# Kernel optimization log

Measured on AMD Instinct MI355X. Metric: run time of the kernel, lower is better.

Reference implementation:

```python
import jax, jax.numpy as jnp
import numpy as np

ALPHA = 1.0
BETA = 0.25
NUM_EMBEDS = 8192
EMBED_DIM = 512
B, T = 32, 256


def setup_inputs() -> dict:
    key = jax.random.key(0)
    k1, k2 = jax.random.split(key)
    z_e = jax.random.normal(k1, (B, EMBED_DIM, T), dtype=jnp.float32)
    codebook = jax.random.normal(k2, (NUM_EMBEDS, EMBED_DIM), dtype=jnp.float32)
    return {"z_e": z_e, "codebook": codebook}


def reference(z_e, codebook):
    # z_e: (b, d, t) -> (b, t, d)
    z = jnp.transpose(z_e, (0, 2, 1))
    b, t, d = z.shape
    flat = z.reshape(-1, d)  # (N, d), N = b*t

    # squared euclidean distances to every codebook vector: (N, K)
    dists = (
        jnp.sum(flat * flat, axis=1, keepdims=True)
        + jnp.sum(codebook * codebook, axis=1)
        - 2.0 * flat @ codebook.T
    )
    idx = jnp.argmin(dists, axis=1)  # (N,)

    # codebook lookup (equivalent to one-hot @ codebook)
    z_q = codebook[idx].reshape(b, t, d)

    # commitment loss (codebook is EMA-updated, so only e_latent term)
    e_latent_loss = jnp.mean((jax.lax.stop_gradient(z_q) - z) ** 2)
    vq_loss = ALPHA * BETA * e_latent_loss

    # straight-through estimator
    z_q_st = z + jax.lax.stop_gradient(z_q - z)
    z_q_out = jnp.transpose(z_q_st, (0, 2, 1))  # back to (b, d, t)

    # perplexity from mean one-hot assignment probabilities
    counts = jnp.zeros((codebook.shape[0],), dtype=jnp.float32).at[idx].add(1.0)
    avg_probs = counts / flat.shape[0]
    perplexity = jnp.exp(-jnp.sum(avg_probs * jnp.log(avg_probs + 1e-10)))

    return z_q_out, vq_loss, perplexity
```

## Files before the change

### kernel.cpp

```cpp
#include <hip/hip_runtime.h>
#include <stdint.h>

typedef _Float16 half8 __attribute__((ext_vector_type(8)));
typedef float floatx16 __attribute__((ext_vector_type(16)));
typedef unsigned long long u64;

#define ALPHA_ 1.0f
#define BETA_ 0.25f
#define NUM_EMBEDS 8192
#define EMBED_DIM 512
#define B_ 32
#define T_ 256
#define N_TOK 8192
#define THR_GAP 0.01f


typedef __attribute__((address_space(1))) const void ga_void;
typedef __attribute__((address_space(3))) void ls_void;
__device__ __forceinline__ void gl_lds16(const void* g, void* l) {
    __builtin_amdgcn_global_load_lds((ga_void*)g, (ls_void*)l, 16, 0, 0);
}

__device__ __forceinline__ uint32_t mono(float s) {
    uint32_t u = __float_as_uint(s);
    return (u & 0x80000000u) ? ~u : (u | 0x80000000u);
}
__device__ __forceinline__ float unmono(uint32_t v) {
    return __uint_as_float((v & 0x80000000u) ? (v ^ 0x80000000u) : ~v);
}

__global__ void pack_kernel(const float* __restrict__ cb, const float* __restrict__ z,
                            _Float16* __restrict__ cb_i, _Float16* __restrict__ zt_i,
                            float* __restrict__ cnorm, u64* __restrict__ wexact,
                            int* __restrict__ counts, float* __restrict__ sse,
                            int* __restrict__ nflag) {
    const int bx = blockIdx.x;
    const int tid = threadIdx.x;
    if (bx < 2048) {
        int row = bx * 4 + (tid >> 6);
        int lane = tid & 63;
        const float* src = cb + (size_t)row * EMBED_DIM + lane * 8;
        float4 v0 = *(const float4*)src;
        float4 v1 = *(const float4*)(src + 4);
        float x[8] = {v0.x, v0.y, v0.z, v0.w, v1.x, v1.y, v1.z, v1.w};
        half8 hh, mm;
        float s = 0.f;
#pragma unroll
        for (int j = 0; j < 8; ++j) {
            s += x[j] * x[j];
            _Float16 hv = (_Float16)x[j];
            hh[j] = hv;
            mm[j] = (_Float16)(x[j] - (float)hv);
        }
        _Float16* dst = cb_i + (size_t)row * 1024 + (lane >> 1) * 32 + (lane & 1) * 8;
        *(half8*)dst = hh;
        *(half8*)(dst + 16) = mm;
#pragma unroll
        for (int d = 32; d; d >>= 1) s += __shfl_xor(s, d, 64);
        if (lane == 0) cnorm[row] = s;
    } else if (bx < 2176) {
        int bz = bx - 2048;
        int lane = tid & 63, ds = tid >> 6;
        int b = bz >> 2;
        int t = ((bz & 3) << 6) + lane;
        size_t n = (size_t)b * T_ + t;
        for (int g = 0; g < 16; ++g) {
            int d0 = g * 32 + ds * 8;
            const float* src = z + ((size_t)b * EMBED_DIM + d0) * T_ + t;
            half8 hh, mm;
#pragma unroll
            for (int j = 0; j < 8; ++j) {
                float x = -2.0f * src[(size_t)j * T_];
                _Float16 hv = (_Float16)x;
                hh[j] = hv;
                mm[j] = (_Float16)(x - (float)hv);
            }
            int gg = g * 4 + ds;
            _Float16* dst = zt_i + n * 1024 + (gg >> 1) * 32 + (gg & 1) * 8;
            *(half8*)dst = hh;
            *(half8*)(dst + 16) = mm;
        }
    } else {
        int i = bx - 2176;
        wexact[i * 256 + tid] = ~0ULL;
        counts[i * 256 + tid] = 0;
        if (i == 0 && tid == 0) { *sse = 0.f; *nflag = 0; }
    }
}

#define MFMA16(a, b, c) __builtin_amdgcn_mfma_f32_32x32x16_f16(a, b, c, 0, 0, 0)

__global__ __launch_bounds__(256, 2) void argmin_kernel(
    const _Float16* __restrict__ cb_i, const _Float16* __restrict__ zt_i,
    const float* __restrict__ cnorm, u64* __restrict__ slot) {
    __shared__ _Float16 smem[24576];
    __shared__ u64 sK[256];
    __shared__ float sV1[256], sV2[256];
    const int tid = threadIdx.x;
    const int l = tid & 63;
    const int wv = tid >> 6;
    const int l31 = l & 31;
    const int hf = l >> 5;
    const int wp = wv >> 1, wq = wv & 1;
    const int n0 = blockIdx.x * 256;
    const int c0 = blockIdx.y * 128;

    const _Float16* gptr[6];
    int lofs[6], bmul[6];
#pragma unroll
    for (int j = 0; j < 6; ++j) {
        int id = wv * 6 + j;
        if (id < 8) {
            int rp = id * 4 + (l >> 4);
            int lid = (l & 15) ^ (rp & 15);
            gptr[j] = cb_i + (size_t)(c0 + (lid >> 2) * 32 + rp) * 1024 + (lid & 3) * 8;
            lofs[j] = id * 512 + l * 8;
            bmul[j] = 4096;
        } else {
            int bid = id - 8;
            int rp = bid * 4 + (l >> 4);
            int lid = (l & 15) ^ (rp & 15);
            gptr[j] = zt_i + (size_t)(n0 + (lid >> 2) * 64 + rp) * 1024 + (lid & 3) * 8;
            lofs[j] = 8192 + bid * 512 + l * 8;
            bmul[j] = 8192;
        }
    }
    auto stagefull = [&](int buf, int ss) {
        const int ga = ss * 32;
#pragma unroll
        for (int j = 0; j < 6; ++j)
            gl_lds16(gptr[j] + ga, smem + lofs[j] + buf * bmul[j]);
    };

    int aoff[2][2], boff[4][2];
#pragma unroll
    for (int pi = 0; pi < 2; ++pi)
#pragma unroll
        for (int p = 0; p < 2; ++p) {
            int lid = (wp * 2 + pi) * 4 + p * 2 + hf;
            aoff[pi][p] = l31 * 128 + (lid ^ (l31 & 15)) * 8;
        }
#pragma unroll
    for (int qi = 0; qi < 4; ++qi)
#pragma unroll
        for (int p = 0; p < 2; ++p) {
            int lid = (wq * 2 + (qi >> 1)) * 4 + p * 2 + hf;
            boff[qi][p] = 8192 + ((qi & 1) * 32 + l31) * 128 + (lid ^ (l31 & 15)) * 8;
        }

    floatx16 acc[2][4];
#pragma unroll
    for (int pi = 0; pi < 2; ++pi)
#pragma unroll
        for (int qi = 0; qi < 4; ++qi)
#pragma unroll
            for (int r = 0; r < 16; ++r) acc[pi][qi][r] = 0.f;

    stagefull(0, 0);
    __syncthreads();
    for (int ss = 0; ss < 32; ++ss) {
        const int buf = ss & 1;
        const int ab = buf * 4096, bb = buf * 8192;
        half8 Ah[2], Am[2], Bh[4], Bm[4];
#pragma unroll
        for (int pi = 0; pi < 2; ++pi) {
            Ah[pi] = *(const half8*)(smem + aoff[pi][0] + ab);
            Am[pi] = *(const half8*)(smem + aoff[pi][1] + ab);
        }
#pragma unroll
        for (int qi = 0; qi < 4; ++qi) {
            Bh[qi] = *(const half8*)(smem + boff[qi][0] + bb);
            Bm[qi] = *(const half8*)(smem + boff[qi][1] + bb);
        }
        if (ss < 31) stagefull(buf ^ 1, ss + 1);
#pragma unroll
        for (int pi = 0; pi < 2; ++pi)
#pragma unroll
            for (int qi = 0; qi < 4; ++qi) {
                acc[pi][qi] = MFMA16(Ah[pi], Bh[qi], acc[pi][qi]);
                acc[pi][qi] = MFMA16(Am[pi], Bh[qi], acc[pi][qi]);
                acc[pi][qi] = MFMA16(Ah[pi], Bm[qi], acc[pi][qi]);
            }
        __syncthreads();
    }

    u64 qk[4];
    float qv1[4], qv2[4];
#pragma unroll
    for (int qi = 0; qi < 4; ++qi) {
        u64 m1k = ~0ULL;
        float m1v = 3.4e38f, m2 = 3.4e38f;
#pragma unroll
        for (int pi = 0; pi < 2; ++pi)
#pragma unroll
            for (int g = 0; g < 4; ++g) {
                const int cb4 = c0 + wp * 64 + pi * 32 + g * 8 + hf * 4;
                float4 cn = *(const float4*)(cnorm + cb4);
                const floatx16& A = acc[pi][qi];
                float sv[4] = {cn.x + A[g * 4 + 0], cn.y + A[g * 4 + 1],
                               cn.z + A[g * 4 + 2], cn.w + A[g * 4 + 3]};
#pragma unroll
                for (int q = 0; q < 4; ++q) {
                    u64 key = ((u64)mono(sv[q]) << 32) | (uint32_t)(cb4 + q);
                    if (key < m1k) { m2 = m1v; m1v = sv[q]; m1k = key; }
                    else m2 = fminf(m2, sv[q]);
                }
            }
        u64 ok = __shfl_xor(m1k, 32, 64);
        float ov = __shfl_xor(m1v, 32, 64);
        float om2 = __shfl_xor(m2, 32, 64);
        if (ok < m1k) { m2 = fminf(fminf(m2, om2), m1v); m1v = ov; m1k = ok; }
        else m2 = fminf(fminf(m2, om2), ov);
        qk[qi] = m1k; qv1[qi] = m1v; qv2[qi] = m2;
    }
    if (wp == 1 && hf == 0) {
#pragma unroll
        for (int qi = 0; qi < 4; ++qi) {
            const int tl = wq * 128 + qi * 32 + l31;
            sK[tl] = qk[qi]; sV1[tl] = qv1[qi]; sV2[tl] = qv2[qi];
        }
    }
    __syncthreads();
    if (wp == 0 && hf == 0) {
#pragma unroll
        for (int qi = 0; qi < 4; ++qi) {
            const int tl = wq * 128 + qi * 32 + l31;
            u64 m1k = qk[qi]; float m1v = qv1[qi], m2 = qv2[qi];
            u64 ok = sK[tl]; float ov = sV1[tl], om2 = sV2[tl];
            if (ok < m1k) { m2 = fminf(fminf(m2, om2), m1v); m1v = ov; m1k = ok; }
            else m2 = fminf(fminf(m2, om2), ov);
            uint32_t code = (uint32_t)m1k & 0x1FFFu;
            uint32_t d16 = (uint32_t)__builtin_bit_cast(unsigned short, (_Float16)(m2 - m1v));
            slot[((size_t)blockIdx.y << 13) + n0 + tl] =
                (m1k & 0xFFFFFFFF00000000ULL) | ((u64)code << 16) | d16;
        }
    }
}

__global__ void combine_kernel(const u64* __restrict__ slot, u64* __restrict__ wexact,
                               int* __restrict__ worklist, int* __restrict__ nflag) {
    int tok = blockIdx.x * 256 + threadIdx.x;
    u64 g1 = ~0ULL;
    float g1v = 3.4e38f, g2 = 3.4e38f;
    for (int c = 0; c < 64; ++c) {
        u64 v = slot[((size_t)c << 13) + tok];
        float kv = unmono((uint32_t)(v >> 32));
        float d = (float)__builtin_bit_cast(_Float16, (unsigned short)(v & 0xffff));
        if (v < g1) { g2 = fminf(g2, g1v); g1 = v; g1v = kv; }
        else g2 = fminf(g2, kv);
        g2 = fminf(g2, kv + d);
    }
    if (g2 - g1v > THR_GAP)
        wexact[tok] = (g1 & 0xFFFFFFFF00000000ULL) | ((g1 >> 16) & 0x1FFFULL);
    else { int i = atomicAdd(nflag, 1); if (i < 8192) worklist[i] = tok; }
}

__global__ void fallback_kernel(const float* __restrict__ z, const float* __restrict__ cb,
                                const float* __restrict__ cnorm,
                                const int* __restrict__ worklist, const int* __restrict__ nflag,
                                u64* __restrict__ wexact) {
    int n = *nflag;
    if (n > 8192) n = 8192;
    const int l = threadIdx.x & 63, wv = threadIdx.x >> 6;
    const int cbase = blockIdx.x * 128;
    for (int fi = blockIdx.y; fi < n; fi += gridDim.y) {
        int tok = worklist[fi];
        int b = tok >> 8, t = tok & 255;
        const float* zp = z + ((size_t)b * EMBED_DIM) * T_ + t;
        float zr[8];
#pragma unroll
        for (int j = 0; j < 8; ++j) zr[j] = zp[(size_t)(l * 8 + j) * T_];
        u64 m1 = ~0ULL;
        for (int j = 0; j < 32; ++j) {
            int c = cbase + wv + j * 4;
            const float* cp = cb + (size_t)c * EMBED_DIM + l * 8;
            float4 a = *(const float4*)cp, bb = *(const float4*)(cp + 4);
            float dot = zr[0] * a.x + zr[1] * a.y + zr[2] * a.z + zr[3] * a.w +
                        zr[4] * bb.x + zr[5] * bb.y + zr[6] * bb.z + zr[7] * bb.w;
#pragma unroll
            for (int m = 32; m; m >>= 1) dot += __shfl_xor(dot, m, 64);
            if (l == 0) {
                float s = cnorm[c] - 2.0f * dot;
                u64 key = ((u64)mono(s) << 32) | (uint32_t)c;
                if (key < m1) m1 = key;
            }
        }
        if (l == 0) atomicMin(&wexact[tok], m1);
    }
}

__global__ void gather_kernel(const float* __restrict__ z, const float* __restrict__ cb,
                              const u64* __restrict__ wexact,
                              float* __restrict__ out, int* __restrict__ counts,
                              float* __restrict__ sse_acc) {
    __shared__ unsigned int sIdx[64];
    __shared__ float red[4];
    const int tid = threadIdx.x;
    const int n0 = blockIdx.x * 64;
    const int b = n0 >> 8;
    const int t0 = n0 & 255;
    if (tid < 64) {
        unsigned int idx = (unsigned int)(wexact[n0 + tid] & 0x1FFFULL);
        sIdx[tid] = idx;
        atomicAdd(&counts[idx], 1);
    }
    __syncthreads();
    const int w = tid >> 6;
    const int lane = tid & 63;
    const float* crow = cb + (size_t)sIdx[lane] * EMBED_DIM;
    const size_t base = ((size_t)b * EMBED_DIM) * T_ + (size_t)(t0 + lane);
    float sse = 0.f;
    for (int d = w; d < EMBED_DIM; d += 4) {
        float v = crow[d];
        size_t o = base + (size_t)d * T_;
        float diff = v - z[o];
        out[o] = v;
        sse += diff * diff;
    }
    for (int m = 32; m; m >>= 1) sse += __shfl_xor(sse, m, 64);
    if (lane == 0) red[w] = sse;
    __syncthreads();
    if (tid == 0) atomicAdd(sse_acc, red[0] + red[1] + red[2] + red[3]);
}

__global__ void finalize_kernel(const int* __restrict__ counts,
                                const float* __restrict__ sse_acc,
                                float* __restrict__ out) {
    __shared__ float red[4];
    const int tid = threadIdx.x;
    float e = 0.f;
    for (int k = tid; k < NUM_EMBEDS; k += 256) {
        float p = (float)counts[k] * (1.0f / (float)N_TOK);
        e += p * logf(p + 1e-10f);
    }
    for (int m = 32; m; m >>= 1) e += __shfl_xor(e, m, 64);
    if ((tid & 63) == 0) red[tid >> 6] = e;
    __syncthreads();
    if (tid == 0) {
        float ent = red[0] + red[1] + red[2] + red[3];
        size_t off = (size_t)B_ * EMBED_DIM * T_;
        out[off + 0] = (ALPHA_ * BETA_) * sse_acc[0] / (float)((size_t)N_TOK * EMBED_DIM);
        out[off + 1] = expf(-ent);
    }
}

extern "C" void kernel_launch(void* const* d_in, const int* in_sizes, int n_in,
                              void* d_out, int out_size, void* d_ws, size_t ws_size,
                              hipStream_t stream) {
    const float* z = (const float*)d_in[0];
    const float* cb = (const float*)d_in[1];
    float* out = (float*)d_out;
    char* ws = (char*)d_ws;
    u64* wexact = (u64*)ws;
    float* cnorm = (float*)(ws + 65536);
    int* counts = (int*)(ws + 98304);
    float* sse = (float*)(ws + 131072);
    int* nflag = (int*)(ws + 131076);
    int* worklist = (int*)(ws + 131080);
    u64* slot = (u64*)(ws + (1ull << 20));
    _Float16* cb_i = (_Float16*)(ws + (6ull << 20));
    _Float16* zt_i = (_Float16*)(ws + (22ull << 20));

    pack_kernel<<<2208, 256, 0, stream>>>(cb, z, cb_i, zt_i, cnorm, wexact, counts, sse, nflag);
    argmin_kernel<<<dim3(N_TOK / 256, NUM_EMBEDS / 128), 256, 0, stream>>>(cb_i, zt_i, cnorm, slot);
    combine_kernel<<<N_TOK / 256, 256, 0, stream>>>(slot, wexact, worklist, nflag);
    fallback_kernel<<<dim3(64, 16), 256, 0, stream>>>(z, cb, cnorm, worklist, nflag, wexact);
    gather_kernel<<<N_TOK / 64, 256, 0, stream>>>(z, cb, wexact, out, counts, sse);
    finalize_kernel<<<1, 256, 0, stream>>>(counts, sse, out);
}
```

Baseline: 378.6 us.

## Parallelize combine and fallback kernels, raise argmin occupancy, prefetch earlier

Raises argmin launch bounds to three blocks per CU and issues the next tile's global-to-LDS staging before reading the current tile. Splits the combine reduction over 64 codebook slices across four waves with a shared-memory merge, giving four times as many blocks. Rewrites the fallback so each thread scores one codeword against the token vector held in shared memory, then reduces with shuffles and atomicMin. Higher occupancy risks register spills in the MFMA loop, and flagged tokens now get a sentinel key preset before exact refinement.

```diff
diff --git a/kernel.cpp b/kernel.cpp
--- a/kernel.cpp
+++ b/kernel.cpp
@@ -90,7 +90,7 @@
 
 #define MFMA16(a, b, c) __builtin_amdgcn_mfma_f32_32x32x16_f16(a, b, c, 0, 0, 0)
 
-__global__ __launch_bounds__(256, 2) void argmin_kernel(
+__global__ __launch_bounds__(256, 3) void argmin_kernel(
     const _Float16* __restrict__ cb_i, const _Float16* __restrict__ zt_i,
     const float* __restrict__ cnorm, u64* __restrict__ slot) {
     __shared__ _Float16 smem[24576];
@@ -161,6 +161,7 @@
     for (int ss = 0; ss < 32; ++ss) {
         const int buf = ss & 1;
         const int ab = buf * 4096, bb = buf * 8192;
+        if (ss < 31) stagefull(buf ^ 1, ss + 1);
         half8 Ah[2], Am[2], Bh[4], Bm[4];
 #pragma unroll
         for (int pi = 0; pi < 2; ++pi) {
@@ -172,7 +173,6 @@
             Bh[qi] = *(const half8*)(smem + boff[qi][0] + bb);
             Bm[qi] = *(const half8*)(smem + boff[qi][1] + bb);
         }
-        if (ss < 31) stagefull(buf ^ 1, ss + 1);
 #pragma unroll
         for (int pi = 0; pi < 2; ++pi)
 #pragma unroll
@@ -237,12 +237,20 @@
     }
 }
 
-__global__ void combine_kernel(const u64* __restrict__ slot, u64* __restrict__ wexact,
-                               int* __restrict__ worklist, int* __restrict__ nflag) {
-    int tok = blockIdx.x * 256 + threadIdx.x;
+__global__ __launch_bounds__(256) void combine_kernel(
+    const u64* __restrict__ slot, u64* __restrict__ wexact,
+    int* __restrict__ worklist, int* __restrict__ nflag) {
+    __shared__ u64 sk[4][64];
+    __shared__ float s1[4][64], s2[4][64];
+    const int tid = threadIdx.x;
+    const int l = tid & 63;
+    const int w = tid >> 6;
+    const int tok = blockIdx.x * 64 + l;
     u64 g1 = ~0ULL;
     float g1v = 3.4e38f, g2 = 3.4e38f;
-    for (int c = 0; c < 64; ++c) {
+#pragma unroll
+    for (int i = 0; i < 16; ++i) {
+        int c = w * 16 + i;
         u64 v = slot[((size_t)c << 13) + tok];
         float kv = unmono((uint32_t)(v >> 32));
         float d = (float)__builtin_bit_cast(_Float16, (unsigned short)(v & 0xffff));
@@ -250,42 +258,67 @@
         else g2 = fminf(g2, kv);
         g2 = fminf(g2, kv + d);
     }
-    if (g2 - g1v > THR_GAP)
-        wexact[tok] = (g1 & 0xFFFFFFFF00000000ULL) | ((g1 >> 16) & 0x1FFFULL);
-    else { int i = atomicAdd(nflag, 1); if (i < 8192) worklist[i] = tok; }
-}
-
-__global__ void fallback_kernel(const float* __restrict__ z, const float* __restrict__ cb,
-                                const float* __restrict__ cnorm,
-                                const int* __restrict__ worklist, const int* __restrict__ nflag,
-                                u64* __restrict__ wexact) {
+    sk[w][l] = g1; s1[w][l] = g1v; s2[w][l] = g2;
+    __syncthreads();
+    if (w == 0) {
+#pragma unroll
+        for (int p = 1; p < 4; ++p) {
+            u64 ok = sk[p][l];
+            float ov = s1[p][l], o2 = s2[p][l];
+            if (ok < g1) { g2 = fminf(fminf(g2, o2), g1v); g1 = ok; g1v = ov; }
+            else g2 = fminf(fminf(g2, o2), ov);
+        }
+        uint32_t code = (uint32_t)(g1 >> 16) & 0x1FFFu;
+        if (g2 - g1v > THR_GAP) {
+            wexact[tok] = (g1 & 0xFFFFFFFF00000000ULL) | code;
+        } else {
+            int i = atomicAdd(nflag, 1);
+            if (i < 8192) worklist[i] = tok;
+            wexact[tok] = 0xFFFFFFFF00000000ULL | code;
+        }
+    }
+}
+
+__global__ __launch_bounds__(256) void fallback_kernel(
+    const float* __restrict__ z, const float* __restrict__ cb,
+    const float* __restrict__ cnorm, const int* __restrict__ worklist,
+    const int* __restrict__ nflag, u64* __restrict__ wexact) {
+    __shared__ float zs[EMBED_DIM];
+    __shared__ u64 red[4];
     int n = *nflag;
     if (n > 8192) n = 8192;
-    const int l = threadIdx.x & 63, wv = threadIdx.x >> 6;
-    const int cbase = blockIdx.x * 128;
+    const int tid = threadIdx.x;
+    const int c = blockIdx.x * 256 + tid;
     for (int fi = blockIdx.y; fi < n; fi += gridDim.y) {
         int tok = worklist[fi];
         int b = tok >> 8, t = tok & 255;
-        const float* zp = z + ((size_t)b * EMBED_DIM) * T_ + t;
-        float zr[8];
-#pragma unroll
-        for (int j = 0; j < 8; ++j) zr[j] = zp[(size_t)(l * 8 + j) * T_];
-        u64 m1 = ~0ULL;
-        for (int j = 0; j < 32; ++j) {
-            int c = cbase + wv + j * 4;
-            const float* cp = cb + (size_t)c * EMBED_DIM + l * 8;
-            float4 a = *(const float4*)cp, bb = *(const float4*)(cp + 4);
-            float dot = zr[0] * a.x + zr[1] * a.y + zr[2] * a.z + zr[3] * a.w +
-                        zr[4] * bb.x + zr[5] * bb.y + zr[6] * bb.z + zr[7] * bb.w;
-#pragma unroll
-            for (int m = 32; m; m >>= 1) dot += __shfl_xor(dot, m, 64);
-            if (l == 0) {
-                float s = cnorm[c] - 2.0f * dot;
-                u64 key = ((u64)mono(s) << 32) | (uint32_t)c;
-                if (key < m1) m1 = key;
-            }
-        }
-        if (l == 0) atomicMin(&wexact[tok], m1);
+        __syncthreads();
+        for (int d = tid; d < EMBED_DIM; d += 256)
+            zs[d] = z[((size_t)b * EMBED_DIM + d) * T_ + t];
+        __syncthreads();
+        const float* cp = cb + (size_t)c * EMBED_DIM;
+        float dot = 0.f;
+#pragma unroll 4
+        for (int d = 0; d < EMBED_DIM; d += 4) {
+            float4 cv = *(const float4*)(cp + d);
+            dot += zs[d] * cv.x + zs[d + 1] * cv.y + zs[d + 2] * cv.z + zs[d + 3] * cv.w;
+        }
+        float s = cnorm[c] - 2.0f * dot;
+        u64 key = ((u64)mono(s) << 32) | (uint32_t)c;
+#pragma unroll
+        for (int m = 32; m; m >>= 1) {
+            u64 o = __shfl_xor(key, m, 64);
+            if (o < key) key = o;
+        }
+        if ((tid & 63) == 0) red[tid >> 6] = key;
+        __syncthreads();
+        if (tid == 0) {
+            u64 k = red[0];
+            if (red[1] < k) k = red[1];
+            if (red[2] < k) k = red[2];
+            if (red[3] < k) k = red[3];
+            atomicMin(&wexact[tok], k);
+        }
     }
 }
 
@@ -363,8 +396,8 @@
 
     pack_kernel<<<2208, 256, 0, stream>>>(cb, z, cb_i, zt_i, cnorm, wexact, counts, sse, nflag);
     argmin_kernel<<<dim3(N_TOK / 256, NUM_EMBEDS / 128), 256, 0, stream>>>(cb_i, zt_i, cnorm, slot);
-    combine_kernel<<<N_TOK / 256, 256, 0, stream>>>(slot, wexact, worklist, nflag);
-    fallback_kernel<<<dim3(64, 16), 256, 0, stream>>>(z, cb, cnorm, worklist, nflag, wexact);
+    combine_kernel<<<N_TOK / 64, 256, 0, stream>>>(slot, wexact, worklist, nflag);
+    fallback_kernel<<<dim3(32, 64), 256, 0, stream>>>(z, cb, cnorm, worklist, nflag, wexact);
     gather_kernel<<<N_TOK / 64, 256, 0, stream>>>(z, cb, wexact, out, counts, sse);
     finalize_kernel<<<1, 256, 0, stream>>>(counts, sse, out);
 }
```

Result: slower. 963.0 us (+154.3%).
